# Optimization experiments

Hardware: AMD Instinct MI355X
Metric: run time of the kernel (lower is better)

Reference implementation:

```python
import jax, jax.numpy as jnp
import numpy as np

NH = 12      # bert-base heads
NL = 32      # num_latents
K = 64       # hard-coded topk in forward


def _ln(x, g, b):
    m = x.mean(-1, keepdims=True)
    v = ((x - m) ** 2).mean(-1, keepdims=True)
    return (x - m) / jnp.sqrt(v + 1e-12) * g + b


def _attn(xq, xkv, w, b, mask_add=None):
    # w: [4,H,H] (q,k,v,o), b: [4,H]
    B, Lq, H = xq.shape
    dh = H // NH
    q = (xq @ w[0] + b[0]).reshape(B, Lq, NH, dh)
    k = (xkv @ w[1] + b[1]).reshape(B, -1, NH, dh)
    v = (xkv @ w[2] + b[2]).reshape(B, -1, NH, dh)
    s = jnp.einsum('bqhd,bkhd->bhqk', q, k) / np.sqrt(dh).astype(xq.dtype)
    if mask_add is not None:
        s = s + mask_add
    p = jax.nn.softmax(s, axis=-1)          # [B,NH,Lq,Lk]
    o = jnp.einsum('bhqk,bkhd->bqhd', p, v).reshape(B, Lq, H)
    return o @ w[3] + b[3], p


def _cross_block(q, enc, w, b, g, lb, mask_add=None):
    # w:[L,8,H,H]; per layer: self-attn+LN then cross-attn+LN (FFN stripped)
    p_last = None
    for l in range(w.shape[0]):
        a, _ = _attn(q, q, w[l, :4], b[l, :4])
        q = _ln(q + a, g[l, 0], lb[l, 0])
        a, p_last = _attn(q, enc, w[l, 4:], b[l, 4:], mask_add)
        q = _ln(q + a, g[l, 1], lb[l, 1])
    return q, p_last


def _self_block(q, w, b, g, lb):
    probs = []
    for l in range(w.shape[0]):
        a, p = _attn(q, q, w[l], b[l])
        q = _ln(q + a, g[l, 0], lb[l, 0])
        probs.append(p)
    return q, jnp.concatenate(probs, axis=1)  # concat over head dim like torch.concat(attentions, dim=1)


def setup_inputs() -> dict:
    key = jax.random.key(0)
    ks = jax.random.split(key, 24)
    B, S, T, H, L = 32, 1024, 64, 768, 2
    std = 0.02
    inp = {
        'audio_embeds': jax.random.normal(ks[0], (B, S, H), jnp.float32),
        'text_embeds': jax.random.normal(ks[1], (B, T, H), jnp.float32),
        'attention_mask': jnp.ones((B, T), jnp.int32),
        'audio_qt': jax.random.normal(ks[2], (1, NL, H), jnp.float32) * std,
        'text_qt': jax.random.normal(ks[3], (1, NL, H), jnp.float32) * std,
    }
    for i, pre in enumerate(['tm', 'am', 'mg']):
        inp[pre + '_w'] = jax.random.normal(ks[4 + i], (L, 8, H, H), jnp.float32) * std
        inp[pre + '_b'] = jnp.zeros((L, 8, H), jnp.float32)
        inp[pre + '_g'] = jnp.ones((L, 2, H), jnp.float32)
        inp[pre + '_lb'] = jnp.zeros((L, 2, H), jnp.float32)
    inp['sel_w'] = jax.random.normal(ks[8], (L, 4, H, H), jnp.float32) * std
    inp['sel_b'] = jnp.zeros((L, 4, H), jnp.float32)
    inp['sel_g'] = jnp.ones((L, 1, H), jnp.float32)
    inp['sel_lb'] = jnp.zeros((L, 1, H), jnp.float32)
    return inp


def reference(audio_embeds, text_embeds, audio_qt, text_qt,
              tm_w, tm_b, tm_g, tm_lb, am_w, am_b, am_g, am_lb,
              sel_w, sel_b, sel_g, sel_lb, mg_w, mg_b, mg_g, mg_lb,
              attention_mask):
    B, S, H = audio_embeds.shape
    mask_add = (1.0 - attention_mask.astype(audio_embeds.dtype))[:, None, None, :] * -1e4

    # text token merger
    latent_text, _ = _cross_block(jnp.broadcast_to(text_qt, (B, NL, H)), text_embeds,
                                  tm_w, tm_b, tm_g, tm_lb, mask_add)
    # audio token merger (capture last-layer cross-attn probs)
    latent_audio, cross_p = _cross_block(jnp.broadcast_to(audio_qt, (B, NL, H)), audio_embeds,
                                         am_w, am_b, am_g, am_lb)
    latent_attention_score = cross_p.mean(axis=1)          # [B,NL,S]

    latent = jnp.concatenate([latent_audio, latent_text], axis=1)  # [B,2NL,H]
    fused, attn_all = _self_block(latent, sel_w, sel_b, sel_g, sel_lb)  # attn_all [B,L*NH,2NL,2NL]
    aas = attn_all[:, :, :NL, NL:].mean(axis=1)            # [B,NL,NL]

    imp = jnp.einsum('bqk,bks->bqs', aas, latent_attention_score).mean(axis=1)  # [B,S]
    _, idx = jax.lax.top_k(imp, K)
    sorted_idx = jnp.sort(idx, axis=1)                     # [B,K]

    sel_mask = jnp.zeros((B, S), bool).at[jnp.arange(B)[:, None], sorted_idx].set(True)
    q_tokens = jnp.take_along_axis(audio_embeds, sorted_idx[..., None], axis=1)  # [B,K,H]
    unsel_idx = jnp.argsort(sel_mask, axis=1, stable=True)[:, :S - K]            # order-preserving
    kv_rest = jnp.take_along_axis(audio_embeds, unsel_idx[..., None], axis=1)    # [B,S-K,H]
    kv = jnp.concatenate([kv_rest, fused], axis=1)                               # [B,S,H]

    out, _ = _cross_block(q_tokens, kv, mg_w, mg_b, mg_g, mg_lb)
    return out
```

## Files before the change

kernel.cpp:

```cpp
#include <hip/hip_runtime.h>
#include <hip/hip_bf16.h>
#include <math.h>

namespace {
constexpr int kB = 32, kS = 1024, kT = 64, kH = 768, kNH = 12, kDH = 64;
constexpr int kNL = 32, kTopK = 64, kL = 2;
constexpr size_t kMat = (size_t)kH * kH;
}

typedef _Float16 half8 __attribute__((ext_vector_type(8)));
typedef float floatx4 __attribute__((ext_vector_type(4)));

#define AS1U(p) ((const __attribute__((address_space(1))) unsigned int*)(p))
#define AS3U(p) ((__attribute__((address_space(3))) unsigned int*)(p))

__device__ __forceinline__ void split_write(float v, _Float16* H, _Float16* L, size_t i) {
    _Float16 h = (_Float16)v;
    H[i] = h;
    L[i] = (_Float16)(v - (float)h);
}

template<int NP>
__global__ __launch_bounds__(256) void gemm16(
    const _Float16* __restrict__ Aqh, const _Float16* __restrict__ Aql,
// ... 16 lines not shown
    _Float16* Oh = (z == 0) ? O0h : (z == 1) ? O1h : O2h;
    _Float16* Ol = (z == 0) ? O0l : (z == 1) ? O1l : O2l;

    constexpr int NPL = (NP == 3) ? 4 : 2;
    __shared__ _Float16 lds[NPL * 4096];
    const int tid = threadIdx.x;
    const int lane = tid & 63, wave = tid >> 6;
    const size_t rm = (size_t)blockIdx.x * 128;
    const size_t cn = (size_t)blockIdx.y * 128;
    const int wr = (wave >> 1) * 64, wc = (wave & 1) * 64;

    const int lrow = lane >> 2;
    const int lchunk = (lane & 3) ^ ((lane >> 3) & 3);
    const int q = lane >> 4;
    const int fr = lane & 15;
    const int rslot = q ^ ((fr >> 1) & 3);

    const _Float16* gsrc;
    _Float16* lbase;
    int jbase;
    if constexpr (NP == 3) {
        gsrc = (wave == 0) ? Ah + rm * kH : (wave == 1) ? Al + rm * kH
             : (wave == 2) ? Bh + cn * kH : Bl + cn * kH;
        lbase = &lds[wave * 4096];
        jbase = 0;
    } else {
        gsrc = (wave < 2) ? Ah + rm * kH : Bh + cn * kH;
        lbase = &lds[(wave >> 1) * 4096];
        jbase = (wave & 1) * 4;
    }
    constexpr int CPW = (NP == 3) ? 8 : 4;

    floatx4 acc[4][4] = {};

    for (int k0 = 0; k0 < kH; k0 += 32) {
        #pragma unroll
        for (int c = 0; c < CPW; ++c) {
            int j = jbase + c;
            const _Float16* src = gsrc + (size_t)(j * 16 + lrow) * kH + k0 + lchunk * 8;
            _Float16* dst = lbase + j * 512 + lane * 8;
            __builtin_amdgcn_global_load_lds(AS1U(src), AS3U(dst), 16, 0, 0);
        }
        __syncthreads();

        half8 ah[4], bh[4], al[4], bl[4];
        #pragma unroll
        for (int m = 0; m < 4; ++m) {
            int r = wr + m * 16 + fr;
            ah[m] = *(const half8*)&lds[r * 32 + rslot * 8];
            if constexpr (NP == 3) al[m] = *(const half8*)&lds[4096 + r * 32 + rslot * 8];
        }
        constexpr int pb = (NP == 3) ? 2 : 1;
        #pragma unroll
        for (int n = 0; n < 4; ++n) {
            int r = wc + n * 16 + fr;
            bh[n] = *(const half8*)&lds[pb * 4096 + r * 32 + rslot * 8];
            if constexpr (NP == 3) bl[n] = *(const half8*)&lds[3 * 4096 + r * 32 + rslot * 8];
        }
        #pragma unroll
        for (int m = 0; m < 4; ++m)
            #pragma unroll
            for (int n = 0; n < 4; ++n) {
                acc[m][n] = __builtin_amdgcn_mfma_f32_16x16x32_f16(ah[m], bh[n], acc[m][n], 0, 0, 0);
                if constexpr (NP == 3) {
                    acc[m][n] = __builtin_amdgcn_mfma_f32_16x16x32_f16(ah[m], bl[n], acc[m][n], 0, 0, 0);
                    acc[m][n] = __builtin_amdgcn_mfma_f32_16x16x32_f16(al[m], bh[n], acc[m][n], 0, 0, 0);
                }
            }
        __syncthreads();
    }
    #pragma unroll
    for (int m = 0; m < 4; ++m) {
        int row0 = wr + m * 16 + (lane >> 4) * 4;
        #pragma unroll
        for (int n = 0; n < 4; ++n) {
            int col = (int)cn + wc + n * 16 + fr;
            float bv = bz[col];
// ... 31 lines not shown
    _Float16* Oh = (z == 0) ? O0h : (z == 1) ? O1h : O2h;
    _Float16* Ol = (z == 0) ? O0l : (z == 1) ? O1l : O2l;

    constexpr int NPL = (NP == 3) ? 4 : 2;
    __shared__ _Float16 lds[NPL * 2048];
    const int tid = threadIdx.x;
    const int lane = tid & 63, wave = tid >> 6;
    const size_t rm = (size_t)blockIdx.x * 64;
    const size_t cn = (size_t)blockIdx.y * 64;
    const int wr = (wave >> 1) * 32, wc = (wave & 1) * 32;

    const int lrow = lane >> 2;
    const int lchunk = (lane & 3) ^ ((lane >> 3) & 3);
    const int q = lane >> 4;
    const int fr = lane & 15;
    const int rslot = q ^ ((fr >> 1) & 3);

    const _Float16* gsrc;
    _Float16* lbase;
    int jbase;
    if constexpr (NP == 3) {
        gsrc = (wave == 0) ? Ah + rm * kH : (wave == 1) ? Al + rm * kH
             : (wave == 2) ? Bh + cn * kH : Bl + cn * kH;
        lbase = &lds[wave * 2048];
        jbase = 0;
    } else {
        gsrc = (wave < 2) ? Ah + rm * kH : Bh + cn * kH;
        lbase = &lds[(wave >> 1) * 2048];
        jbase = (wave & 1) * 2;
    }
    constexpr int CPW = (NP == 3) ? 4 : 2;

    floatx4 acc[2][2] = {};

    for (int k0 = 0; k0 < kH; k0 += 32) {
        #pragma unroll
        for (int c = 0; c < CPW; ++c) {
            int j = jbase + c;
            const _Float16* src = gsrc + (size_t)(j * 16 + lrow) * kH + k0 + lchunk * 8;
            _Float16* dst = lbase + j * 512 + lane * 8;
            __builtin_amdgcn_global_load_lds(AS1U(src), AS3U(dst), 16, 0, 0);
        }
        __syncthreads();

        half8 ah[2], bh[2], al[2], bl[2];
        #pragma unroll
        for (int m = 0; m < 2; ++m) {
            int r = wr + m * 16 + fr;
            ah[m] = *(const half8*)&lds[r * 32 + rslot * 8];
            if constexpr (NP == 3) al[m] = *(const half8*)&lds[2048 + r * 32 + rslot * 8];
        }
        constexpr int pb = (NP == 3) ? 2 : 1;
        #pragma unroll
        for (int n = 0; n < 2; ++n) {
            int r = wc + n * 16 + fr;
            bh[n] = *(const half8*)&lds[pb * 2048 + r * 32 + rslot * 8];
            if constexpr (NP == 3) bl[n] = *(const half8*)&lds[3 * 2048 + r * 32 + rslot * 8];
        }
        #pragma unroll
        for (int m = 0; m < 2; ++m)
            #pragma unroll
            for (int n = 0; n < 2; ++n) {
                acc[m][n] = __builtin_amdgcn_mfma_f32_16x16x32_f16(ah[m], bh[n], acc[m][n], 0, 0, 0);
                if constexpr (NP == 3) {
                    acc[m][n] = __builtin_amdgcn_mfma_f32_16x16x32_f16(ah[m], bl[n], acc[m][n], 0, 0, 0);
                    acc[m][n] = __builtin_amdgcn_mfma_f32_16x16x32_f16(al[m], bh[n], acc[m][n], 0, 0, 0);
                }
            }
        __syncthreads();
    }
    #pragma unroll
    for (int m = 0; m < 2; ++m) {
        int row0 = wr + m * 16 + (lane >> 4) * 4;
        #pragma unroll
        for (int n = 0; n < 2; ++n) {
            int col = (int)cn + wc + n * 16 + fr;
            float bv = bz[col];
// ... 61 lines not shown
            ah[m] = *(const half8*)&lds[r * 32 + rslot * 8];
            if constexpr (NP == 3) al[m] = *(const half8*)&lds[2048 + r * 32 + rslot * 8];
        }
        constexpr int pb = (NP == 3) ? 2 : 1;
        #pragma unroll
        for (int n = 0; n < 2; ++n) {
            int r = wc + n * 16 + fr;
            bh[n] = *(const half8*)&lds[pb * 2048 + r * 32 + rslot * 8];
            if constexpr (NP == 3) bl[n] = *(const half8*)&lds[3 * 2048 + r * 32 + rslot * 8];
        }
        #pragma unroll
        for (int m = 0; m < 2; ++m)
            #pragma unroll
            for (int n = 0; n < 2; ++n) {
                acc[m][n] = __builtin_amdgcn_mfma_f32_16x16x32_f16(ah[m], bh[n], acc[m][n], 0, 0, 0);
                if constexpr (NP == 3) {
                    acc[m][n] = __builtin_amdgcn_mfma_f32_16x16x32_f16(ah[m], bl[n], acc[m][n], 0, 0, 0);
                    acc[m][n] = __builtin_amdgcn_mfma_f32_16x16x32_f16(al[m], bh[n], acc[m][n], 0, 0, 0);
                }
            }
        __syncthreads();
    }
    #pragma unroll
    for (int m = 0; m < 2; ++m) {
        int row0 = wr + m * 16 + (lane >> 4) * 4;
        #pragma unroll
        for (int n = 0; n < 2; ++n) {
            int col = (int)cn + wc + n * 16 + fr;
            float bv = bias[col];
            #pragma unroll
            for (int j = 0; j < 4; ++j)
                Y[(rm + row0 + j) * (size_t)kH + col] = acc[m][n][j] + bv;
        }
    }
}

template<int NP>
__global__ __launch_bounds__(256) void attn_big(
    const _Float16* __restrict__ Qh, const _Float16* __restrict__ Ql,
    const _Float16* __restrict__ Kh, const _Float16* __restrict__ Kl,
    float* __restrict__ P, int Lq, int Lk)
{
    constexpr int NPL = (NP == 3) ? 2 : 1;
    const int tid = threadIdx.x, lane = tid & 63, wave = tid >> 6;
    const int fr = lane & 15, part = lane >> 4;
    const int bh = blockIdx.x, b = bh / kNH, h = bh % kNH;
    const int q0 = blockIdx.y * 32;
    const int key0 = wave * 256;
    __shared__ float red[32][4];

    half8 qa[2][2][NPL];
    #pragma unroll
    for (int m = 0; m < 2; ++m)
        #pragma unroll
        for (int c = 0; c < 2; ++c) {
            size_t ro = (size_t)(b * Lq + q0 + m * 16 + fr) * kH + h * kDH + c * 32 + part * 8;
            qa[m][c][0] = *(const half8*)&Qh[ro];
            if constexpr (NP == 3) qa[m][c][1] = *(const half8*)&Ql[ro];
        }
    floatx4 acc[2][16] = {};
    #pragma unroll
    for (int n = 0; n < 16; ++n)
        #pragma unroll
        for (int c = 0; c < 2; ++c) {
            size_t ro = (size_t)(b * Lk + key0 + n * 16 + fr) * kH + h * kDH + c * 32 + part * 8;
            half8 kh8 = *(const half8*)&Kh[ro];
// ... 462 lines not shown
    for (int c = threadIdx.x; c < kH; c += 256)
        split_write(src[c], Kh, Kl, (size_t)br * kH + c);
}

extern "C" void kernel_launch(void* const* d_in, const int* in_sizes, int n_in,
                              void* d_out, int out_size, void* d_ws, size_t ws_size,
                              hipStream_t stream)
{
    const float* audio    = (const float*)d_in[0];
    const float* text     = (const float*)d_in[1];
    const int*   amask    = (const int*)  d_in[2];
    const float* audio_qt = (const float*)d_in[3];
    const float* text_qt  = (const float*)d_in[4];
    const float* tm_w  = (const float*)d_in[5];
    const float* tm_b  = (const float*)d_in[6];
    const float* tm_g  = (const float*)d_in[7];
    const float* tm_lb = (const float*)d_in[8];
    const float* am_w  = (const float*)d_in[9];
    const float* am_b  = (const float*)d_in[10];
    const float* am_g  = (const float*)d_in[11];
    const float* am_lb = (const float*)d_in[12];
    const float* mg_w  = (const float*)d_in[13];
    const float* mg_b  = (const float*)d_in[14];
    const float* mg_g  = (const float*)d_in[15];
    const float* mg_lb = (const float*)d_in[16];
    const float* sel_w  = (const float*)d_in[17];
    const float* sel_b  = (const float*)d_in[18];
    const float* sel_g  = (const float*)d_in[19];
    const float* sel_lb = (const float*)d_in[20];
    (void)in_sizes; (void)n_in; (void)out_size;

    char* base = (char*)d_ws;
    size_t off = 0;
    auto alloc = [&](size_t bytes) {
        off = (off + 255) & ~(size_t)255;
        void* p = base + off; off += bytes; return p;
    };
    float* Pbuf   = (float*)alloc((size_t)kB * kNH * 64 * kS * 4);
    float* attA   = (float*)alloc((size_t)2048 * kH * 4);
    float* q_text = (float*)alloc((size_t)1024 * kH * 4);
    float* q_audio= (float*)alloc((size_t)1024 * kH * 4);
    float* latent = (float*)alloc((size_t)2048 * kH * 4);
    float* qmerge = (float*)alloc((size_t)2048 * kH * 4);
    float* latsc  = (float*)alloc((size_t)kB * kNL * kS * 4);
    float* aas    = (float*)alloc((size_t)kB * kNL * kNL * 4);
    float* impb   = (float*)alloc((size_t)kB * kS * 4);
    int* selidx   = (int*)alloc((size_t)kB * kTopK * 4);
    int* unselidx = (int*)alloc((size_t)kB * (kS - kTopK) * 4);
    _Float16* Wh  = (_Float16*)alloc(16 * kMat * 2);
    _Float16* Wl  = (_Float16*)alloc(16 * kMat * 2);
    _Float16* BGh = (_Float16*)alloc((size_t)kB * kS * kH * 2);
    _Float16* BGl = (_Float16*)alloc((size_t)kB * kS * kH * 2);
    _Float16* PTh = (_Float16*)alloc((size_t)kB * kT * kH * 2);
    _Float16* PTl = (_Float16*)alloc((size_t)kB * kT * kH * 2);
    _Float16* PLqh= (_Float16*)alloc((size_t)2048 * kH * 2);
    _Float16* PLql= (_Float16*)alloc((size_t)2048 * kH * 2);
    _Float16* PLoh= (_Float16*)alloc((size_t)2048 * kH * 2);
    _Float16* PLol= (_Float16*)alloc((size_t)2048 * kH * 2);
    _Float16* KVh = (_Float16*)alloc((size_t)kB * kS * kH * 2);
    _Float16* KVl = (_Float16*)alloc((size_t)kB * kS * kH * 2);
    if (off > ws_size) return;

    _Float16* Qh = PLoh;
    _Float16* Ql = PLol;

    auto attn = [&](const float* qf, int Lq,
                    const _Float16* qah, const _Float16* qal,
                    const _Float16* eah, const _Float16* eal, int Lk,
                    int wmat, const float* bias, const float* g, const float* lb,
                    const int* mask, int capture, bool np3,
                    float* q_out, _Float16* oh, _Float16* ol)
    {
        const int Mq = kB * Lq, Mk = kB * Lk;
        const _Float16* WhB = Wh + (size_t)wmat * kMat;
        const _Float16* WlB = Wl + (size_t)wmat * kMat;
        if (Lk >= 256) {
            const int gx = Mk / 128;
            dim3 g1(gx, 6, 2);
            if (np3) gemm16<3><<<g1, 256, 0, stream>>>(qah, qal, eah, eal, WhB, WlB, bias,
                         Qh, Ql, KVh, KVl, nullptr, nullptr, Mq, Mk);
            else     gemm16<1><<<g1, 256, 0, stream>>>(qah, qal, eah, eal, WhB, WlB, bias,
                         Qh, Ql, KVh, KVl, nullptr, nullptr, Mq, Mk);
            dim3 g2(kB * kNH, Lq / 32);
            if (np3) attn_big<3><<<g2, 256, 0, stream>>>(Qh, Ql, KVh, KVl, Pbuf, Lq, Lk);
            else     attn_big<1><<<g2, 256, 0, stream>>>(Qh, Ql, KVh, KVl, Pbuf, Lq, Lk);
            if (capture == 1) mean_heads<<<kB * kNL, 256, 0, stream>>>(Pbuf, latsc);
            dim3 g3(Mk / 128, 6, 1);
            if (np3) gemm16<3><<<g3, 256, 0, stream>>>(eah, eal, eah, eal,
                         WhB + 2 * kMat, WlB + 2 * kMat, bias + 2 * kH,
                         KVh, KVl, nullptr, nullptr, nullptr, nullptr, Mk, Mk);
            else     gemm16<1><<<g3, 256, 0, stream>>>(eah, eal, eah, eal,
                         WhB + 2 * kMat, WlB + 2 * kMat, bias + 2 * kH,
                         KVh, KVl, nullptr, nullptr, nullptr, nullptr, Mk, Mk);
            if (Lq == 32) {
                if (np3) pv_mfma<32, 3><<<kB * kNH, 128, 0, stream>>>(Pbuf, KVh, KVl, PLoh, PLol, Lk);
                else     pv_mfma<32, 1><<<kB * kNH, 128, 0, stream>>>(Pbuf, KVh, KVl, PLoh, PLol, Lk);
            } else {
                if (np3) pv_mfma<64, 3><<<kB * kNH, 256, 0, stream>>>(Pbuf, KVh, KVl, PLoh, PLol, Lk);
                else     pv_mfma<64, 1><<<kB * kNH, 256, 0, stream>>>(Pbuf, KVh, KVl, PLoh, PLol, Lk);
            }
        } else {
            _Float16* V2h = KVh + (size_t)Mk * kH;
            _Float16* V2l = KVl + (size_t)Mk * kH;
            const int gx = (Mq > Mk ? Mq : Mk) / 64;
            dim3 g1(gx, 12, 3);
            if (np3) gemm16s<3><<<g1, 256, 0, stream>>>(qah, qal, eah, eal, WhB, WlB, bias,
                         Qh, Ql, KVh, KVl, V2h, V2l, Mq, Mk);
            else     gemm16s<1><<<g1, 256, 0, stream>>>(qah, qal, eah, eal, WhB, WlB, bias,
                         Qh, Ql, KVh, KVl, V2h, V2l, Mq, Mk);
            if (Lq == 32 && Lk == 32)
                attn_small<32, 32, 3, false, false><<<kB * kNH, 128, 0, stream>>>(
                    Qh, Ql, KVh, KVl, V2h, V2l, PLoh, PLol, nullptr, nullptr);
            else if (Lq == 32 && Lk == 64)
                attn_small<32, 64, 3, true, false><<<kB * kNH, 128, 0, stream>>>(
                    Qh, Ql, KVh, KVl, V2h, V2l, PLoh, PLol, nullptr, mask);
            else if (np3)
                attn_small<64, 64, 3, false, true><<<kB * kNH, 256, 0, stream>>>(
                    Qh, Ql, KVh, KVl, V2h, V2l, PLoh, PLol, Pbuf, nullptr);
            else
                attn_small<64, 64, 1, false, false><<<kB * kNH, 256, 0, stream>>>(
                    Qh, Ql, KVh, KVl, V2h, V2l, PLoh, PLol, nullptr, nullptr);
            if (capture == 2)      aas_acc<<<kB, 256, 0, stream>>>(Pbuf, aas, 1);
            else if (capture == 3) aas_acc<<<kB, 256, 0, stream>>>(Pbuf, aas, 0);
        }
        dim3 g4(Mq / 64, 12);
        if (np3) gemm_o32s<3><<<g4, 256, 0, stream>>>(PLoh, PLol, WhB + 3 * kMat, WlB + 3 * kMat,
                     bias + 3 * kH, attA, Mq);
        else     gemm_o32s<1><<<g4, 256, 0, stream>>>(PLoh, PLol, WhB + 3 * kMat, WlB + 3 * kMat,
                     bias + 3 * kH, attA, Mq);
        ln_residual<<<Mq, 256, 0, stream>>>(qf, attA, g, lb, q_out, oh, ol);
    };

    split2<<<(kB * kT * kH) / 1024, 256, 0, stream>>>(text, PTh, PTl, kB * kT * kH);
    split2<<<(kB * kS * kH) / 1024, 256, 0, stream>>>(audio, BGh, BGl, kB * kS * kH);

    wconv<<<dim3(24, 24, 16), 256, 0, stream>>>(tm_w, Wh, Wl);
    bcast_q<<<kB * kNL, 256, 0, stream>>>(text_qt, q_text, PLqh, PLql);
    for (int l = 0; l < kL; ++l) {
        attn(q_text, kNL, PLqh, PLql, PLqh, PLql, kNL, l * 8 + 0,
             tm_b + (size_t)l * 8 * kH, tm_g + (size_t)l * 2 * kH, tm_lb + (size_t)l * 2 * kH,
             nullptr, 0, true, q_text, PLqh, PLql);
        attn(q_text, kNL, PLqh, PLql, PTh, PTl, kT, l * 8 + 4,
             tm_b + ((size_t)l * 8 + 4) * kH, tm_g + ((size_t)l * 2 + 1) * kH, tm_lb + ((size_t)l * 2 + 1) * kH,
             amask, 0, true, q_text, PLqh, PLql);
    }
    wconv<<<dim3(24, 24, 16), 256, 0, stream>>>(am_w, Wh, Wl);
    bcast_q<<<kB * kNL, 256, 0, stream>>>(audio_qt, q_audio, PLqh, PLql);
    for (int l = 0; l < kL; ++l) {
        attn(q_audio, kNL, PLqh, PLql, PLqh, PLql, kNL, l * 8 + 0,
             am_b + (size_t)l * 8 * kH, am_g + (size_t)l * 2 * kH, am_lb + (size_t)l * 2 * kH,
             nullptr, 0, true, q_audio, PLqh, PLql);
        attn(q_audio, kNL, PLqh, PLql, BGh, BGl, kS, l * 8 + 4,
             am_b + ((size_t)l * 8 + 4) * kH, am_g + ((size_t)l * 2 + 1) * kH, am_lb + ((size_t)l * 2 + 1) * kH,
             nullptr, (l == kL - 1) ? 1 : 0, true, q_audio, PLqh, PLql);
    }
    concat_lat<<<kB * 64, 256, 0, stream>>>(q_audio, q_text, latent, PLqh, PLql);
    wconv<<<dim3(24, 24, 8), 256, 0, stream>>>(sel_w, Wh, Wl);
    for (int l = 0; l < kL; ++l) {
        attn(latent, 64, PLqh, PLql, PLqh, PLql, 64, l * 4,
             sel_b + (size_t)l * 4 * kH, sel_g + (size_t)l * kH, sel_lb + (size_t)l * kH,
             nullptr, (l == 0) ? 2 : 3, true, latent, PLqh, PLql);
    }
    imp_kernel<<<kB, 256, 0, stream>>>(aas, latsc, impb);
    topk_kernel<<<kB, 256, 0, stream>>>(impb, selidx, unselidx);
    gather_q<<<kB * kTopK, 256, 0, stream>>>(audio, selidx, qmerge, PLqh, PLql);
    build_kv<<<kB * kS, 256, 0, stream>>>(audio, latent, unselidx, BGh, BGl);
    wconv<<<dim3(24, 24, 16), 256, 0, stream>>>(mg_w, Wh, Wl);
    for (int l = 0; l < kL; ++l) {
        attn(qmerge, 64, PLqh, PLql, PLqh, PLql, 64, l * 8 + 0,
             mg_b + (size_t)l * 8 * kH, mg_g + (size_t)l * 2 * kH, mg_lb + (size_t)l * 2 * kH,
             nullptr, 0, false, qmerge, PLqh, PLql);
        float* qo = (l == kL - 1) ? (float*)d_out : qmerge;
        _Float16* oh = (l == kL - 1) ? nullptr : PLqh;
        _Float16* ol = (l == kL - 1) ? nullptr : PLql;
        attn(qmerge, 64, PLqh, PLql, BGh, BGl, kS, l * 8 + 4,
             mg_b + ((size_t)l * 8 + 4) * kH, mg_g + ((size_t)l * 2 + 1) * kH, mg_lb + ((size_t)l * 2 + 1) * kH,
             nullptr, 0, false, qo, oh, ol);
    }
}
```

Measured before the change: 2.107 ms.

## Factor cross-attention through weights to avoid projecting long K/V sequences

For the long-sequence cross-attention layers (audio and merge blocks), the key projection is folded into the query: per head, R = Q_h·Wk_hᵀ is computed and then scored directly against the raw encoder embeddings. The probabilities are multiplied by the transposed raw embeddings, and the value projection is applied afterwards on the small per-head result. This removes the large K and V projection GEMMs over 32x1024 tokens. In exchange it adds a transpose of the encoder input, per-head Lq×768 intermediates, and a new batched GEMM, softmax and output-GEMM path. The key bias is dropped, which is valid because it only shifts each score row by a constant under softmax. A fallback keeps the old path when the workspace is too small.

```diff
diff --git a/kernel.cpp b/kernel.cpp
--- a/kernel.cpp
+++ b/kernel.cpp
@@ -72,7 +72,6 @@
     constexpr int CPW = (NP == 3) ? 8 : 4;
 
     floatx4 acc[4][4] = {};
-
     for (int k0 = 0; k0 < kH; k0 += 32) {
         #pragma unroll
         for (int c = 0; c < CPW; ++c) {
@@ -82,7 +81,6 @@
             __builtin_amdgcn_global_load_lds(AS1U(src), AS3U(dst), 16, 0, 0);
         }
         __syncthreads();
-
         half8 ah[4], bh[4], al[4], bl[4];
         #pragma unroll
         for (int m = 0; m < 4; ++m) {
@@ -180,7 +178,6 @@
     constexpr int CPW = (NP == 3) ? 4 : 2;
 
     floatx4 acc[2][2] = {};
-
     for (int k0 = 0; k0 < kH; k0 += 32) {
         #pragma unroll
         for (int c = 0; c < CPW; ++c) {
@@ -190,7 +187,6 @@
             __builtin_amdgcn_global_load_lds(AS1U(src), AS3U(dst), 16, 0, 0);
         }
         __syncthreads();
-
         half8 ah[2], bh[2], al[2], bl[2];
         #pragma unroll
         for (int m = 0; m < 2; ++m) {
@@ -318,6 +314,294 @@
             for (int j = 0; j < 4; ++j)
                 Y[(rm + row0 + j) * (size_t)kH + col] = acc[m][n][j] + bv;
         }
+    }
+}
+
+template<int NP, int KD, bool OUT16>
+__global__ __launch_bounds__(256) void gemmB(
+    const _Float16* __restrict__ Ah, const _Float16* __restrict__ Al,
+    const _Float16* __restrict__ Bh, const _Float16* __restrict__ Bl,
+    float scale, float* __restrict__ O32,
+    _Float16* __restrict__ O16h, _Float16* __restrict__ O16l,
+    int M, int N)
+{
+    const int b = blockIdx.z;
+    const _Float16* Ahb = Ah + (size_t)b * M * KD;
+    const _Float16* Alb = Al + (size_t)b * M * KD;
+    const _Float16* Bhb = Bh + (size_t)b * N * KD;
+    const _Float16* Blb = Bl + (size_t)b * N * KD;
+
+    constexpr int NPL = (NP == 3) ? 4 : 2;
+    __shared__ _Float16 lds[NPL * 4096];
+    const int tid = threadIdx.x;
+    const int lane = tid & 63, wave = tid >> 6;
+    const size_t rm = (size_t)blockIdx.x * 128;
+    const size_t cn = (size_t)blockIdx.y * 128;
+    const int wr = (wave >> 1) * 64, wc = (wave & 1) * 64;
+
+    const int lrow = lane >> 2;
+    const int lchunk = (lane & 3) ^ ((lane >> 3) & 3);
+    const int q = lane >> 4;
+    const int fr = lane & 15;
+    const int rslot = q ^ ((fr >> 1) & 3);
+
+    const _Float16* gsrc;
+    _Float16* lbase;
+    int jbase;
+    if constexpr (NP == 3) {
+        gsrc = (wave == 0) ? Ahb + rm * KD : (wave == 1) ? Alb + rm * KD
+             : (wave == 2) ? Bhb + cn * KD : Blb + cn * KD;
+        lbase = &lds[wave * 4096];
+        jbase = 0;
+    } else {
+        gsrc = (wave < 2) ? Ahb + rm * KD : Bhb + cn * KD;
+        lbase = &lds[(wave >> 1) * 4096];
+        jbase = (wave & 1) * 4;
+    }
+    constexpr int CPW = (NP == 3) ? 8 : 4;
+
+    floatx4 acc[4][4] = {};
+    for (int k0 = 0; k0 < KD; k0 += 32) {
+        #pragma unroll
+        for (int c = 0; c < CPW; ++c) {
+            int j = jbase + c;
+            const _Float16* src = gsrc + (size_t)(j * 16 + lrow) * KD + k0 + lchunk * 8;
+            _Float16* dst = lbase + j * 512 + lane * 8;
+            __builtin_amdgcn_global_load_lds(AS1U(src), AS3U(dst), 16, 0, 0);
+        }
+        __syncthreads();
+        half8 ah[4], bh[4], al[4], bl[4];
+        #pragma unroll
+        for (int m = 0; m < 4; ++m) {
+            int r = wr + m * 16 + fr;
+            ah[m] = *(const half8*)&lds[r * 32 + rslot * 8];
+            if constexpr (NP == 3) al[m] = *(const half8*)&lds[4096 + r * 32 + rslot * 8];
+        }
+        constexpr int pb = (NP == 3) ? 2 : 1;
+        #pragma unroll
+        for (int n = 0; n < 4; ++n) {
+            int r = wc + n * 16 + fr;
+            bh[n] = *(const half8*)&lds[pb * 4096 + r * 32 + rslot * 8];
+            if constexpr (NP == 3) bl[n] = *(const half8*)&lds[3 * 4096 + r * 32 + rslot * 8];
+        }
+        #pragma unroll
+        for (int m = 0; m < 4; ++m)
+            #pragma unroll
+            for (int n = 0; n < 4; ++n) {
+                acc[m][n] = __builtin_amdgcn_mfma_f32_16x16x32_f16(ah[m], bh[n], acc[m][n], 0, 0, 0);
+                if constexpr (NP == 3) {
+                    acc[m][n] = __builtin_amdgcn_mfma_f32_16x16x32_f16(ah[m], bl[n], acc[m][n], 0, 0, 0);
+                    acc[m][n] = __builtin_amdgcn_mfma_f32_16x16x32_f16(al[m], bh[n], acc[m][n], 0, 0, 0);
+                }
+            }
+        __syncthreads();
+    }
+    const size_t ob = (size_t)b * M * N;
+    #pragma unroll
+    for (int m = 0; m < 4; ++m) {
+        int row0 = wr + m * 16 + (lane >> 4) * 4;
+        #pragma unroll
+        for (int n = 0; n < 4; ++n) {
+            int col = (int)cn + wc + n * 16 + fr;
+            #pragma unroll
+            for (int j = 0; j < 4; ++j) {
+                float v = acc[m][n][j] * scale;
+                size_t oi = ob + (rm + row0 + j) * (size_t)N + col;
+                if constexpr (OUT16) {
+                    _Float16 hh = (_Float16)v;
+                    O16h[oi] = hh;
+                    if constexpr (NP == 3) O16l[oi] = (_Float16)(v - (float)hh);
+                } else {
+                    O32[oi] = v;
+                }
+            }
+        }
+    }
+}
+
+template<int LQ, int NP>
+__global__ __launch_bounds__(256) void rgemm(
+    const _Float16* __restrict__ Qh, const _Float16* __restrict__ Ql,
+    const _Float16* __restrict__ Wnh, const _Float16* __restrict__ Wnl,
+    _Float16* __restrict__ Rh, _Float16* __restrict__ Rl)
+{
+    constexpr int MM = LQ / 16;
+    const int tid = threadIdx.x, lane = tid & 63, wave = tid >> 6;
+    const int fr = lane & 15, part = lane >> 4;
+    const int bh = blockIdx.x, b = bh / kNH, h = bh % kNH;
+    const int ncol = blockIdx.y * 64 + wave * 16;
+
+    half8 qa[MM][2][2];
+    #pragma unroll
+    for (int m = 0; m < MM; ++m)
+        #pragma unroll
+        for (int c = 0; c < 2; ++c) {
+            size_t ro = (size_t)(b * LQ + m * 16 + fr) * kH + h * kDH + c * 32 + part * 8;
+            qa[m][c][0] = *(const half8*)&Qh[ro];
+            if constexpr (NP == 3) qa[m][c][1] = *(const half8*)&Ql[ro];
+        }
+    floatx4 acc[MM] = {};
+    #pragma unroll
+    for (int c = 0; c < 2; ++c) {
+        size_t ro = (size_t)(ncol + fr) * kH + h * kDH + c * 32 + part * 8;
+        half8 wb = *(const half8*)&Wnh[ro];
+        half8 wl;
+        if constexpr (NP == 3) wl = *(const half8*)&Wnl[ro];
+        #pragma unroll
+        for (int m = 0; m < MM; ++m) {
+            acc[m] = __builtin_amdgcn_mfma_f32_16x16x32_f16(qa[m][c][0], wb, acc[m], 0, 0, 0);
+            if constexpr (NP == 3) {
+                acc[m] = __builtin_amdgcn_mfma_f32_16x16x32_f16(qa[m][c][0], wl, acc[m], 0, 0, 0);
+                acc[m] = __builtin_amdgcn_mfma_f32_16x16x32_f16(qa[m][c][1], wb, acc[m], 0, 0, 0);
+            }
+        }
+    }
+    #pragma unroll
+    for (int m = 0; m < MM; ++m)
+        #pragma unroll
+        for (int j = 0; j < 4; ++j) {
+            size_t oi = (size_t)(bh * LQ + m * 16 + part * 4 + j) * kH + ncol + fr;
+            float v = acc[m][j];
+            _Float16 hh = (_Float16)v;
+            Rh[oi] = hh;
+            if constexpr (NP == 3) Rl[oi] = (_Float16)(v - (float)hh);
+        }
+}
+
+template<int LQ, int NP>
+__global__ __launch_bounds__(256) void ogemm(
+    const _Float16* __restrict__ Zh, const _Float16* __restrict__ Zl,
+    const _Float16* __restrict__ WTh, const _Float16* __restrict__ WTl,
+    const float* __restrict__ bv,
+    _Float16* __restrict__ Oh, _Float16* __restrict__ Ol)
+{
+    constexpr int MM = LQ / 16;
+    const int tid = threadIdx.x, lane = tid & 63, wave = tid >> 6;
+    const int fr = lane & 15, part = lane >> 4;
+    const int bh = blockIdx.x, b = bh / kNH, h = bh % kNH;
+    const int colbase = h * kDH + wave * 16;
+
+    floatx4 acc[MM] = {};
+    for (int c = 0; c < 24; ++c) {
+        size_t wo = (size_t)(colbase + fr) * kH + c * 32 + part * 8;
+        half8 wb = *(const half8*)&WTh[wo];
+        half8 wl;
+        if constexpr (NP == 3) wl = *(const half8*)&WTl[wo];
+        #pragma unroll
+        for (int m = 0; m < MM; ++m) {
+            size_t ro = (size_t)(bh * LQ + m * 16 + fr) * kH + c * 32 + part * 8;
+            half8 ah = *(const half8*)&Zh[ro];
+            acc[m] = __builtin_amdgcn_mfma_f32_16x16x32_f16(ah, wb, acc[m], 0, 0, 0);
+            if constexpr (NP == 3) {
+                half8 al = *(const half8*)&Zl[ro];
+                acc[m] = __builtin_amdgcn_mfma_f32_16x16x32_f16(ah, wl, acc[m], 0, 0, 0);
+                acc[m] = __builtin_amdgcn_mfma_f32_16x16x32_f16(al, wb, acc[m], 0, 0, 0);
+            }
+        }
+    }
+    float bias = bv[colbase + fr];
+    #pragma unroll
+    for (int m = 0; m < MM; ++m)
+        #pragma unroll
+        for (int j = 0; j < 4; ++j) {
+            size_t oi = (size_t)(b * LQ + m * 16 + part * 4 + j) * kH + colbase + fr;
+            float v = acc[m][j] + bias;
+            _Float16 hh = (_Float16)v;
+            Oh[oi] = hh;
+            if constexpr (NP == 3) Ol[oi] = (_Float16)(v - (float)hh);
+        }
+}
+
+template<int NPLN>
+__global__ __launch_bounds__(256) void xpose(const _Float16* __restrict__ Xh,
+    const _Float16* __restrict__ Xl, _Float16* __restrict__ Th, _Float16* __restrict__ Tl)
+{
+    __shared__ _Float16 t[2][32][33];
+    const int b = blockIdx.z, e0 = blockIdx.x * 32, k0 = blockIdx.y * 32;
+    const int tid = threadIdx.x;
+    #pragma unroll
+    for (int i = 0; i < 4; ++i) {
+        int idx = tid + i * 256, r = idx >> 5, c = idx & 31;
+        t[0][r][c] = Xh[((size_t)b * kS + k0 + r) * kH + e0 + c];
+        if constexpr (NPLN == 2) t[1][r][c] = Xl[((size_t)b * kS + k0 + r) * kH + e0 + c];
+    }
+    __syncthreads();
+    #pragma unroll
+    for (int i = 0; i < 4; ++i) {
+        int idx = tid + i * 256, r = idx >> 5, c = idx & 31;
+        Th[((size_t)b * kH + e0 + r) * kS + k0 + c] = t[0][c][r];
+        if constexpr (NPLN == 2) Tl[((size_t)b * kH + e0 + r) * kS + k0 + c] = t[1][c][r];
+    }
+}
+
+template<int NP, bool CAP>
+__global__ __launch_bounds__(256) void softmax_f32(float* __restrict__ S,
+    _Float16* __restrict__ Ph, _Float16* __restrict__ Pl, int nrows)
+{
+    const int row = blockIdx.x * 4 + (threadIdx.x >> 6);
+    if (row >= nrows) return;
+    const int lane = threadIdx.x & 63;
+    float* s = S + (size_t)row * kS;
+    float v[16];
+    #pragma unroll
+    for (int i = 0; i < 4; ++i) {
+        float4 x = *(const float4*)&s[i * 256 + lane * 4];
+        v[i * 4] = x.x; v[i * 4 + 1] = x.y; v[i * 4 + 2] = x.z; v[i * 4 + 3] = x.w;
+    }
+    float mx = v[0];
+    #pragma unroll
+    for (int i = 1; i < 16; ++i) mx = fmaxf(mx, v[i]);
+    #pragma unroll
+    for (int o = 1; o < 64; o <<= 1) mx = fmaxf(mx, __shfl_xor(mx, o));
+    float sum = 0.f;
+    #pragma unroll
+    for (int i = 0; i < 16; ++i) { v[i] = expf(v[i] - mx); sum += v[i]; }
+    #pragma unroll
+    for (int o = 1; o < 64; o <<= 1) sum += __shfl_xor(sum, o);
+    float inv = 1.0f / sum;
+    #pragma unroll
+    for (int i = 0; i < 4; ++i)
+        #pragma unroll
+        for (int j = 0; j < 4; ++j) {
+            int idx = i * 256 + lane * 4 + j;
+            float p = v[i * 4 + j] * inv;
+            if constexpr (CAP) s[idx] = p;
+            _Float16 hh = (_Float16)p;
+            Ph[(size_t)row * kS + idx] = hh;
+            if constexpr (NP == 3) Pl[(size_t)row * kS + idx] = (_Float16)(p - (float)hh);
+        }
+}
+
+__global__ __launch_bounds__(256) void softmax_f16k(_Float16* __restrict__ S, int nrows)
+{
+    const int row = blockIdx.x * 4 + (threadIdx.x >> 6);
+    if (row >= nrows) return;
+    const int lane = threadIdx.x & 63;
+    _Float16* s = S + (size_t)row * kS;
+    float v[16];
+    #pragma unroll
+    for (int i = 0; i < 2; ++i) {
+        half8 x = *(const half8*)&s[i * 512 + lane * 8];
+        #pragma unroll
+        for (int j = 0; j < 8; ++j) v[i * 8 + j] = (float)x[j];
+    }
+    float mx = v[0];
+    #pragma unroll
+    for (int i = 1; i < 16; ++i) mx = fmaxf(mx, v[i]);
+    #pragma unroll
+    for (int o = 1; o < 64; o <<= 1) mx = fmaxf(mx, __shfl_xor(mx, o));
+    float sum = 0.f;
+    #pragma unroll
+    for (int i = 0; i < 16; ++i) { v[i] = expf(v[i] - mx); sum += v[i]; }
+    #pragma unroll
+    for (int o = 1; o < 64; o <<= 1) sum += __shfl_xor(sum, o);
+    float inv = 1.0f / sum;
+    #pragma unroll
+    for (int i = 0; i < 2; ++i) {
+        half8 o8;
+        #pragma unroll
+        for (int j = 0; j < 8; ++j) o8[j] = (_Float16)(v[i * 8 + j] * inv);
+        *(half8*)&s[i * 512 + lane * 8] = o8;
     }
 }
 
@@ -846,34 +1130,59 @@
 
     char* base = (char*)d_ws;
     size_t off = 0;
-    auto alloc = [&](size_t bytes) {
+    auto A = [&](size_t bytes) {
         off = (off + 255) & ~(size_t)255;
         void* p = base + off; off += bytes; return p;
     };
-    float* Pbuf   = (float*)alloc((size_t)kB * kNH * 64 * kS * 4);
-    float* attA   = (float*)alloc((size_t)2048 * kH * 4);
-    float* q_text = (float*)alloc((size_t)1024 * kH * 4);
-    float* q_audio= (float*)alloc((size_t)1024 * kH * 4);
-    float* latent = (float*)alloc((size_t)2048 * kH * 4);
-    float* qmerge = (float*)alloc((size_t)2048 * kH * 4);
-    float* latsc  = (float*)alloc((size_t)kB * kNL * kS * 4);
-    float* aas    = (float*)alloc((size_t)kB * kNL * kNL * 4);
-    float* impb   = (float*)alloc((size_t)kB * kS * 4);
-    int* selidx   = (int*)alloc((size_t)kB * kTopK * 4);
-    int* unselidx = (int*)alloc((size_t)kB * (kS - kTopK) * 4);
-    _Float16* Wh  = (_Float16*)alloc(16 * kMat * 2);
-    _Float16* Wl  = (_Float16*)alloc(16 * kMat * 2);
-    _Float16* BGh = (_Float16*)alloc((size_t)kB * kS * kH * 2);
-    _Float16* BGl = (_Float16*)alloc((size_t)kB * kS * kH * 2);
-    _Float16* PTh = (_Float16*)alloc((size_t)kB * kT * kH * 2);
-    _Float16* PTl = (_Float16*)alloc((size_t)kB * kT * kH * 2);
-    _Float16* PLqh= (_Float16*)alloc((size_t)2048 * kH * 2);
-    _Float16* PLql= (_Float16*)alloc((size_t)2048 * kH * 2);
-    _Float16* PLoh= (_Float16*)alloc((size_t)2048 * kH * 2);
-    _Float16* PLol= (_Float16*)alloc((size_t)2048 * kH * 2);
-    _Float16* KVh = (_Float16*)alloc((size_t)kB * kS * kH * 2);
-    _Float16* KVl = (_Float16*)alloc((size_t)kB * kS * kH * 2);
-    if (off > ws_size) return;
+
+    float *Pbuf, *attA, *q_text, *q_audio, *latent, *qmerge, *latsc, *aas, *impb;
+    int *selidx, *unselidx;
+    _Float16 *Wh, *Wl, *WkNh, *WkNl, *BGh, *BGl, *PTh, *PTl;
+    _Float16 *PLqh, *PLql, *PLoh, *PLol, *KVh, *KVl, *XTh, *XTl, *RPreg;
+
+    auto alloc_common = [&]() {
+        attA   = (float*)A((size_t)2048 * kH * 4);
+        q_text = (float*)A((size_t)1024 * kH * 4);
+        q_audio= (float*)A((size_t)1024 * kH * 4);
+        latent = (float*)A((size_t)2048 * kH * 4);
+        qmerge = (float*)A((size_t)2048 * kH * 4);
+        latsc  = (float*)A((size_t)kB * kNL * kS * 4);
+        aas    = (float*)A((size_t)kB * kNL * kNL * 4);
+        impb   = (float*)A((size_t)kB * kS * 4);
+        selidx = (int*)A((size_t)kB * kTopK * 4);
+        unselidx = (int*)A((size_t)kB * (kS - kTopK) * 4);
+        Wh = (_Float16*)A(16 * kMat * 2);
+        Wl = (_Float16*)A(16 * kMat * 2);
+        BGh = (_Float16*)A((size_t)kB * kS * kH * 2);
+        BGl = (_Float16*)A((size_t)kB * kS * kH * 2);
+        PTh = (_Float16*)A((size_t)kB * kT * kH * 2);
+        PTl = (_Float16*)A((size_t)kB * kT * kH * 2);
+        PLqh = (_Float16*)A((size_t)2048 * kH * 2);
+        PLql = (_Float16*)A((size_t)2048 * kH * 2);
+        PLoh = (_Float16*)A((size_t)2048 * kH * 2);
+        PLol = (_Float16*)A((size_t)2048 * kH * 2);
+    };
+
+    off = 0;
+    Pbuf = (float*)A((size_t)kB * kNH * kNL * kS * 4);
+    alloc_common();
+    WkNh = (_Float16*)A(2 * kMat * 2);
+    WkNl = (_Float16*)A(2 * kMat * 2);
+    KVh = (_Float16*)A((size_t)2 * 2048 * kH * 2);
+    KVl = (_Float16*)A((size_t)2 * 2048 * kH * 2);
+    XTh = (_Float16*)A((size_t)kB * kH * kS * 2);
+    XTl = (_Float16*)A((size_t)kB * kH * kS * 2);
+    RPreg = (_Float16*)A((size_t)kB * 768 * kS * 2);
+    bool fact = (off <= ws_size);
+    if (!fact) {
+        off = 0;
+        Pbuf = (float*)A((size_t)kB * kNH * 64 * kS * 4);
+        alloc_common();
+        KVh = (_Float16*)A((size_t)kB * kS * kH * 2);
+        KVl = (_Float16*)A((size_t)kB * kS * kH * 2);
+        WkNh = WkNl = XTh = XTl = RPreg = nullptr;
+        if (off > ws_size) return;
+    }
 
     _Float16* Qh = PLoh;
     _Float16* Ql = PLol;
@@ -888,55 +1197,28 @@
         const int Mq = kB * Lq, Mk = kB * Lk;
         const _Float16* WhB = Wh + (size_t)wmat * kMat;
         const _Float16* WlB = Wl + (size_t)wmat * kMat;
-        if (Lk >= 256) {
-            const int gx = Mk / 128;
-            dim3 g1(gx, 6, 2);
-            if (np3) gemm16<3><<<g1, 256, 0, stream>>>(qah, qal, eah, eal, WhB, WlB, bias,
-                         Qh, Ql, KVh, KVl, nullptr, nullptr, Mq, Mk);
-            else     gemm16<1><<<g1, 256, 0, stream>>>(qah, qal, eah, eal, WhB, WlB, bias,
-                         Qh, Ql, KVh, KVl, nullptr, nullptr, Mq, Mk);
-            dim3 g2(kB * kNH, Lq / 32);
-            if (np3) attn_big<3><<<g2, 256, 0, stream>>>(Qh, Ql, KVh, KVl, Pbuf, Lq, Lk);
-            else     attn_big<1><<<g2, 256, 0, stream>>>(Qh, Ql, KVh, KVl, Pbuf, Lq, Lk);
-            if (capture == 1) mean_heads<<<kB * kNL, 256, 0, stream>>>(Pbuf, latsc);
-            dim3 g3(Mk / 128, 6, 1);
-            if (np3) gemm16<3><<<g3, 256, 0, stream>>>(eah, eal, eah, eal,
-                         WhB + 2 * kMat, WlB + 2 * kMat, bias + 2 * kH,
-                         KVh, KVl, nullptr, nullptr, nullptr, nullptr, Mk, Mk);
-            else     gemm16<1><<<g3, 256, 0, stream>>>(eah, eal, eah, eal,
-                         WhB + 2 * kMat, WlB + 2 * kMat, bias + 2 * kH,
-                         KVh, KVl, nullptr, nullptr, nullptr, nullptr, Mk, Mk);
-            if (Lq == 32) {
-                if (np3) pv_mfma<32, 3><<<kB * kNH, 128, 0, stream>>>(Pbuf, KVh, KVl, PLoh, PLol, Lk);
-                else     pv_mfma<32, 1><<<kB * kNH, 128, 0, stream>>>(Pbuf, KVh, KVl, PLoh, PLol, Lk);
-            } else {
-                if (np3) pv_mfma<64, 3><<<kB * kNH, 256, 0, stream>>>(Pbuf, KVh, KVl, PLoh, PLol, Lk);
-                else     pv_mfma<64, 1><<<kB * kNH, 256, 0, stream>>>(Pbuf, KVh, KVl, PLoh, PLol, Lk);
-            }
-        } else {
-            _Float16* V2h = KVh + (size_t)Mk * kH;
-            _Float16* V2l = KVl + (size_t)Mk * kH;
-            const int gx = (Mq > Mk ? Mq : Mk) / 64;
-            dim3 g1(gx, 12, 3);
-            if (np3) gemm16s<3><<<g1, 256, 0, stream>>>(qah, qal, eah, eal, WhB, WlB, bias,
-                         Qh, Ql, KVh, KVl, V2h, V2l, Mq, Mk);
-            else     gemm16s<1><<<g1, 256, 0, stream>>>(qah, qal, eah, eal, WhB, WlB, bias,
-                         Qh, Ql, KVh, KVl, V2h, V2l, Mq, Mk);
-            if (Lq == 32 && Lk == 32)
-                attn_small<32, 32, 3, false, false><<<kB * kNH, 128, 0, stream>>>(
-                    Qh, Ql, KVh, KVl, V2h, V2l, PLoh, PLol, nullptr, nullptr);
-            else if (Lq == 32 && Lk == 64)
-                attn_small<32, 64, 3, true, false><<<kB * kNH, 128, 0, stream>>>(
-                    Qh, Ql, KVh, KVl, V2h, V2l, PLoh, PLol, nullptr, mask);
-            else if (np3)
-                attn_small<64, 64, 3, false, true><<<kB * kNH, 256, 0, stream>>>(
-                    Qh, Ql, KVh, KVl, V2h, V2l, PLoh, PLol, Pbuf, nullptr);
-            else
-                attn_small<64, 64, 1, false, false><<<kB * kNH, 256, 0, stream>>>(
-                    Qh, Ql, KVh, KVl, V2h, V2l, PLoh, PLol, nullptr, nullptr);
-            if (capture == 2)      aas_acc<<<kB, 256, 0, stream>>>(Pbuf, aas, 1);
-            else if (capture == 3) aas_acc<<<kB, 256, 0, stream>>>(Pbuf, aas, 0);
-        }
+        _Float16* V2h = KVh + (size_t)Mk * kH;
+        _Float16* V2l = KVl + (size_t)Mk * kH;
+        const int gx = (Mq > Mk ? Mq : Mk) / 64;
+        dim3 g1(gx, 12, 3);
+        if (np3) gemm16s<3><<<g1, 256, 0, stream>>>(qah, qal, eah, eal, WhB, WlB, bias,
+                     Qh, Ql, KVh, KVl, V2h, V2l, Mq, Mk);
+        else     gemm16s<1><<<g1, 256, 0, stream>>>(qah, qal, eah, eal, WhB, WlB, bias,
+                     Qh, Ql, KVh, KVl, V2h, V2l, Mq, Mk);
+        if (Lq == 32 && Lk == 32)
+            attn_small<32, 32, 3, false, false><<<kB * kNH, 128, 0, stream>>>(
+                Qh, Ql, KVh, KVl, V2h, V2l, PLoh, PLol, nullptr, nullptr);
+        else if (Lq == 32 && Lk == 64)
+            attn_small<32, 64, 3, true, false><<<kB * kNH, 128, 0, stream>>>(
+                Qh, Ql, KVh, KVl, V2h, V2l, PLoh, PLol, nullptr, mask);
+        else if (np3)
+            attn_small<64, 64, 3, false, true><<<kB * kNH, 256, 0, stream>>>(
+                Qh, Ql, KVh, KVl, V2h, V2l, PLoh, PLol, Pbuf, nullptr);
+        else
+            attn_small<64, 64, 1, false, false><<<kB * kNH, 256, 0, stream>>>(
+                Qh, Ql, KVh, KVl, V2h, V2l, PLoh, PLol, nullptr, nullptr);
+        if (capture == 2)      aas_acc<<<kB, 256, 0, stream>>>(Pbuf, aas, 1);
+        else if (capture == 3) aas_acc<<<kB, 256, 0, stream>>>(Pbuf, aas, 0);
         dim3 g4(Mq / 64, 12);
         if (np3) gemm_o32s<3><<<g4, 256, 0, stream>>>(PLoh, PLol, WhB + 3 * kMat, WlB + 3 * kMat,
                      bias + 3 * kH, attA, Mq);
@@ -945,8 +1227,108 @@
         ln_residual<<<Mq, 256, 0, stream>>>(qf, attA, g, lb, q_out, oh, ol);
     };
 
+    auto big_fact = [&](const float* qf, int Lq,
+                        const _Float16* qah, const _Float16* qal,
+                        int wmat, int kl, const float* bias,
+                        const float* g, const float* lb,
+                        int capture, bool np3,
+                        float* q_out, _Float16* oh, _Float16* ol)
+    {
+        const int Mq = kB * Lq;
+        const int MR = kNH * Lq;
+        const _Float16* WhB = Wh + (size_t)wmat * kMat;
+        const _Float16* WlB = Wl + (size_t)wmat * kMat;
+        dim3 gq(Mq / 64, 12, 1);
+        if (np3) gemm16s<3><<<gq, 256, 0, stream>>>(qah, qal, qah, qal, WhB, WlB, bias,
+                     Qh, Ql, nullptr, nullptr, nullptr, nullptr, Mq, Mq);
+        else     gemm16s<1><<<gq, 256, 0, stream>>>(qah, qal, qah, qal, WhB, WlB, bias,
+                     Qh, Ql, nullptr, nullptr, nullptr, nullptr, Mq, Mq);
+        const _Float16* WKh = WkNh + (size_t)kl * kMat;
+        const _Float16* WKl = WkNl + (size_t)kl * kMat;
+        const int nrows = kB * MR;
+        if (np3) {
+            _Float16* Rh = RPreg;
+            _Float16* Rl = RPreg + (size_t)kB * MR * kH;
+            rgemm<32, 3><<<dim3(kB * kNH, 12), 256, 0, stream>>>(Qh, Ql, WKh, WKl, Rh, Rl);
+            gemmB<3, 768, false><<<dim3(MR / 128, kS / 128, kB), 256, 0, stream>>>(
+                Rh, Rl, BGh, BGl, 0.125f, Pbuf, nullptr, nullptr, MR, kS);
+            _Float16* Ph = RPreg;
+            _Float16* Pl = RPreg + (size_t)kB * MR * kS;
+            if (capture == 1) softmax_f32<3, true><<<(nrows + 3) / 4, 256, 0, stream>>>(Pbuf, Ph, Pl, nrows);
+            else              softmax_f32<3, false><<<(nrows + 3) / 4, 256, 0, stream>>>(Pbuf, Ph, Pl, nrows);
+            if (capture == 1) mean_heads<<<kB * kNL, 256, 0, stream>>>(Pbuf, latsc);
+            _Float16* Zh = (_Float16*)Pbuf;
+            _Float16* Zl = Zh + (size_t)kB * MR * kH;
+            gemmB<3, 1024, true><<<dim3(MR / 128, kH / 128, kB), 256, 0, stream>>>(
+                Ph, Pl, XTh, XTl, 1.0f, nullptr, Zh, Zl, MR, kH);
+            ogemm<32, 3><<<kB * kNH, 256, 0, stream>>>(Zh, Zl, WhB + 2 * kMat, WlB + 2 * kMat,
+                bias + 2 * kH, PLoh, PLol);
+        } else {
+            _Float16* Rh = RPreg;
+            rgemm<64, 1><<<dim3(kB * kNH, 12), 256, 0, stream>>>(Qh, Ql, WKh, WKl, Rh, Rh);
+            _Float16* S16 = (_Float16*)Pbuf;
+            gemmB<1, 768, true><<<dim3(MR / 128, kS / 128, kB), 256, 0, stream>>>(
+                Rh, Rh, BGh, BGh, 0.125f, nullptr, S16, nullptr, MR, kS);
+            softmax_f16k<<<(nrows + 3) / 4, 256, 0, stream>>>(S16, nrows);
+            _Float16* Zh = RPreg;
+            gemmB<1, 1024, true><<<dim3(MR / 128, kH / 128, kB), 256, 0, stream>>>(
+                S16, S16, XTh, XTh, 1.0f, nullptr, Zh, nullptr, MR, kH);
+            ogemm<64, 1><<<kB * kNH, 256, 0, stream>>>(Zh, Zh, WhB + 2 * kMat, WlB + 2 * kMat,
+                bias + 2 * kH, PLoh, PLol);
+        }
+        dim3 g4(Mq / 64, 12);
+        if (np3) gemm_o32s<3><<<g4, 256, 0, stream>>>(PLoh, PLol, WhB + 3 * kMat, WlB + 3 * kMat,
+                     bias + 3 * kH, attA, Mq);
+        else     gemm_o32s<1><<<g4, 256, 0, stream>>>(PLoh, PLol, WhB + 3 * kMat, WlB + 3 * kMat,
+                     bias + 3 * kH, attA, Mq);
+        ln_residual<<<Mq, 256, 0, stream>>>(qf, attA, g, lb, q_out, oh, ol);
+    };
+
+    auto big_fb = [&](const float* qf, int Lq,
+                      const _Float16* qah, const _Float16* qal,
+                      const _Float16* eah, const _Float16* eal,
+                      int wmat, const float* bias, const float* g, const float* lb,
+                      int capture, bool np3,
+                      float* q_out, _Float16* oh, _Float16* ol)
+    {
+        const int Mq = kB * Lq, Mk = kB * kS;
+        const _Float16* WhB = Wh + (size_t)wmat * kMat;
+        const _Float16* WlB = Wl + (size_t)wmat * kMat;
+        const int gx = Mk / 128;
+        dim3 g1(gx, 6, 2);
+        if (np3) gemm16<3><<<g1, 256, 0, stream>>>(qah, qal, eah, eal, WhB, WlB, bias,
+                     Qh, Ql, KVh, KVl, nullptr, nullptr, Mq, Mk);
+        else     gemm16<1><<<g1, 256, 0, stream>>>(qah, qal, eah, eal, WhB, WlB, bias,
+                     Qh, Ql, KVh, KVl, nullptr, nullptr, Mq, Mk);
+        dim3 g2(kB * kNH, Lq / 32);
+        if (np3) attn_big<3><<<g2, 256, 0, stream>>>(Qh, Ql, KVh, KVl, Pbuf, Lq, kS);
+        else     attn_big<1><<<g2, 256, 0, stream>>>(Qh, Ql, KVh, KVl, Pbuf, Lq, kS);
+        if (capture == 1) mean_heads<<<kB * kNL, 256, 0, stream>>>(Pbuf, latsc);
+        dim3 g3(Mk / 128, 6, 1);
+        if (np3) gemm16<3><<<g3, 256, 0, stream>>>(eah, eal, eah, eal,
+                     WhB + 2 * kMat, WlB + 2 * kMat, bias + 2 * kH,
+                     KVh, KVl, nullptr, nullptr, nullptr, nullptr, Mk, Mk);
+        else     gemm16<1><<<g3, 256, 0, stream>>>(eah, eal, eah, eal,
+                     WhB + 2 * kMat, WlB + 2 * kMat, bias + 2 * kH,
+                     KVh, KVl, nullptr, nullptr, nullptr, nullptr, Mk, Mk);
+        if (Lq == 32) {
+            if (np3) pv_mfma<32, 3><<<kB * kNH, 128, 0, stream>>>(Pbuf, KVh, KVl, PLoh, PLol, kS);
+            else     pv_mfma<32, 1><<<kB * kNH, 128, 0, stream>>>(Pbuf, KVh, KVl, PLoh, PLol, kS);
+        } else {
+            if (np3) pv_mfma<64, 3><<<kB * kNH, 256, 0, stream>>>(Pbuf, KVh, KVl, PLoh, PLol, kS);
+            else     pv_mfma<64, 1><<<kB * kNH, 256, 0, stream>>>(Pbuf, KVh, KVl, PLoh, PLol, kS);
+        }
+        dim3 g4(Mq / 64, 12);
+        if (np3) gemm_o32s<3><<<g4, 256, 0, stream>>>(PLoh, PLol, WhB + 3 * kMat, WlB + 3 * kMat,
+                     bias + 3 * kH, attA, Mq);
+        else     gemm_o32s<1><<<g4, 256, 0, stream>>>(PLoh, PLol, WhB + 3 * kMat, WlB + 3 * kMat,
+                     bias + 3 * kH, attA, Mq);
+        ln_residual<<<Mq, 256, 0, stream>>>(qf, attA, g, lb, q_out, oh, ol);
+    };
+
     split2<<<(kB * kT * kH) / 1024, 256, 0, stream>>>(text, PTh, PTl, kB * kT * kH);
     split2<<<(kB * kS * kH) / 1024, 256, 0, stream>>>(audio, BGh, BGl, kB * kS * kH);
+    if (fact) xpose<2><<<dim3(24, 32, 32), 256, 0, stream>>>(BGh, BGl, XTh, XTl);
 
     wconv<<<dim3(24, 24, 16), 256, 0, stream>>>(tm_w, Wh, Wl);
     bcast_q<<<kB * kNL, 256, 0, stream>>>(text_qt, q_text, PLqh, PLql);
@@ -959,14 +1341,23 @@
              amask, 0, true, q_text, PLqh, PLql);
     }
     wconv<<<dim3(24, 24, 16), 256, 0, stream>>>(am_w, Wh, Wl);
+    if (fact)
+        for (int l = 0; l < kL; ++l)
+            split2<<<(int)(kMat / 1024), 256, 0, stream>>>(am_w + ((size_t)l * 8 + 5) * kMat,
+                WkNh + (size_t)l * kMat, WkNl + (size_t)l * kMat, (int)kMat);
     bcast_q<<<kB * kNL, 256, 0, stream>>>(audio_qt, q_audio, PLqh, PLql);
     for (int l = 0; l < kL; ++l) {
         attn(q_audio, kNL, PLqh, PLql, PLqh, PLql, kNL, l * 8 + 0,
              am_b + (size_t)l * 8 * kH, am_g + (size_t)l * 2 * kH, am_lb + (size_t)l * 2 * kH,
              nullptr, 0, true, q_audio, PLqh, PLql);
-        attn(q_audio, kNL, PLqh, PLql, BGh, BGl, kS, l * 8 + 4,
-             am_b + ((size_t)l * 8 + 4) * kH, am_g + ((size_t)l * 2 + 1) * kH, am_lb + ((size_t)l * 2 + 1) * kH,
-             nullptr, (l == kL - 1) ? 1 : 0, true, q_audio, PLqh, PLql);
+        if (fact)
+            big_fact(q_audio, kNL, PLqh, PLql, l * 8 + 4, l,
+                am_b + ((size_t)l * 8 + 4) * kH, am_g + ((size_t)l * 2 + 1) * kH, am_lb + ((size_t)l * 2 + 1) * kH,
+                (l == kL - 1) ? 1 : 0, true, q_audio, PLqh, PLql);
+        else
+            big_fb(q_audio, kNL, PLqh, PLql, BGh, BGl, l * 8 + 4,
+                am_b + ((size_t)l * 8 + 4) * kH, am_g + ((size_t)l * 2 + 1) * kH, am_lb + ((size_t)l * 2 + 1) * kH,
+                (l == kL - 1) ? 1 : 0, true, q_audio, PLqh, PLql);
     }
     concat_lat<<<kB * 64, 256, 0, stream>>>(q_audio, q_text, latent, PLqh, PLql);
     wconv<<<dim3(24, 24, 8), 256, 0, stream>>>(sel_w, Wh, Wl);
@@ -979,7 +1370,12 @@
     topk_kernel<<<kB, 256, 0, stream>>>(impb, selidx, unselidx);
     gather_q<<<kB * kTopK, 256, 0, stream>>>(audio, selidx, qmerge, PLqh, PLql);
     build_kv<<<kB * kS, 256, 0, stream>>>(audio, latent, unselidx, BGh, BGl);
+    if (fact) xpose<1><<<dim3(24, 32, 32), 256, 0, stream>>>(BGh, BGh, XTh, XTh);
     wconv<<<dim3(24, 24, 16), 256, 0, stream>>>(mg_w, Wh, Wl);
+    if (fact)
+        for (int l = 0; l < kL; ++l)
+            split2<<<(int)(kMat / 1024), 256, 0, stream>>>(mg_w + ((size_t)l * 8 + 5) * kMat,
+                WkNh + (size_t)l * kMat, WkNl + (size_t)l * kMat, (int)kMat);
     for (int l = 0; l < kL; ++l) {
         attn(qmerge, 64, PLqh, PLql, PLqh, PLql, 64, l * 8 + 0,
              mg_b + (size_t)l * 8 * kH, mg_g + (size_t)l * 2 * kH, mg_lb + (size_t)l * 2 * kH,
@@ -987,8 +1383,13 @@
         float* qo = (l == kL - 1) ? (float*)d_out : qmerge;
         _Float16* oh = (l == kL - 1) ? nullptr : PLqh;
         _Float16* ol = (l == kL - 1) ? nullptr : PLql;
-        attn(qmerge, 64, PLqh, PLql, BGh, BGl, kS, l * 8 + 4,
-             mg_b + ((size_t)l * 8 + 4) * kH, mg_g + ((size_t)l * 2 + 1) * kH, mg_lb + ((size_t)l * 2 + 1) * kH,
-             nullptr, 0, false, qo, oh, ol);
-    }
-}
+        if (fact)
+            big_fact(qmerge, 64, PLqh, PLql, l * 8 + 4, l,
+                mg_b + ((size_t)l * 8 + 4) * kH, mg_g + ((size_t)l * 2 + 1) * kH, mg_lb + ((size_t)l * 2 + 1) * kH,
+                0, false, qo, oh, ol);
+        else
+            big_fb(qmerge, 64, PLqh, PLql, BGh, BGl, l * 8 + 4,
+                mg_b + ((size_t)l * 8 + 4) * kH, mg_g + ((size_t)l * 2 + 1) * kH, mg_lb + ((size_t)l * 2 + 1) * kH,
+                0, false, qo, oh, ol);
+    }
+}
```

After: 2.109 ms. No clear change (+0.1%).
